# Kernel tuning notes

Hardware: AMD Instinct MI355X
Metric: run time of the kernel (lower is better)

Reference implementation:

```python
import jax, jax.numpy as jnp
import numpy as np


def setup_inputs() -> dict:
    key = jax.random.key(0)
    k1, k2, k3 = jax.random.split(key, 3)
    B, C_in, H, W = 16, 256, 64, 64
    C_out, KH, KW = 256, 3, 3
    x = jax.random.normal(k1, (B, C_in, H, W), dtype=jnp.float32)
    # kaiming-uniform-like scale for realism
    fan_in = C_in * KH * KW
    bound = 1.0 / np.sqrt(fan_in)
    weights = jax.random.normal(k2, (C_out, C_in, KH, KW), dtype=jnp.float32) * bound
    bias = jax.random.uniform(k3, (C_out,), dtype=jnp.float32, minval=-bound, maxval=bound)
    return {"x": x, "weights": weights, "bias": bias}


def reference(x, weights, bias):
    # Conv2dApproximation with approximation_enable=False is an exact conv2d:
    # input is unfolded to [B, C*kh*kw, oh, ow], weights to [C_out, C*kh*kw],
    # and the MultiApp kernel performs the exact MAC (see exact matmul backward).
    # stride=(1,1), padding=(0,0), dilation=(1,1) per init_kwargs.
    out = jax.lax.conv_general_dilated(
        x, weights,
        window_strides=(1, 1),
        padding=((0, 0), (0, 0)),
        rhs_dilation=(1, 1),
        dimension_numbers=("NCHW", "OIHW", "NCHW"),
    )
    return out + bias[None, :, None, None]
```

## Files before the change

### kernel.cpp

```cpp
#include <hip/hip_runtime.h>
#include <stdint.h>

typedef short short8 __attribute__((ext_vector_type(8)));
typedef float f32x4 __attribute__((ext_vector_type(4)));

#define AS1 __attribute__((address_space(1)))
#define AS3 __attribute__((address_space(3)))

__device__ __forceinline__ void gl_lds16(const void* g, void* l) {
  __builtin_amdgcn_global_load_lds((const AS1 unsigned int*)g,
                                   (AS3 unsigned int*)l, 16, 0, 0);
}

__device__ __forceinline__ unsigned short f2bf(float f) {
  union { float f; unsigned int u; } v; v.f = f;
  return (unsigned short)((v.u + (((v.u >> 16) & 1u) + 0x7fffu)) >> 16);
}

__global__ __launch_bounds__(256) void xpose_kernel(const float* __restrict__ x,
                                                    unsigned short* __restrict__ xt) {
  __shared__ float tile[64][68];
  const int bid = blockIdx.x;
  const int cchunk = bid & 3;
  const int y = (bid >> 2) & 63;
  const int b = bid >> 8;
  const int t = threadIdx.x;
  const int ci0 = cchunk * 64;

  const int cc = t >> 2;
  const int xo = (t & 3) * 16;
  const float* src = x + (((size_t)(b * 256 + ci0 + cc) * 64 + y) * 64 + xo);
  float4 v0 = ((const float4*)src)[0];
  float4 v1 = ((const float4*)src)[1];
  float4 v2 = ((const float4*)src)[2];
  float4 v3 = ((const float4*)src)[3];
  *(float4*)&tile[cc][xo + 0]  = v0;
  *(float4*)&tile[cc][xo + 4]  = v1;
  *(float4*)&tile[cc][xo + 8]  = v2;
  *(float4*)&tile[cc][xo + 12] = v3;
  __syncthreads();

  const int xpos = t >> 2;
  const int ccg = (t & 3) * 16;
  unsigned int pk[8];
#pragma unroll
  for (int e = 0; e < 8; ++e) {
    unsigned int lo = f2bf(tile[ccg + 2 * e][xpos]);
    unsigned int hi = f2bf(tile[ccg + 2 * e + 1][xpos]);
    pk[e] = lo | (hi << 16);
  }
  unsigned short* dst = xt + ((size_t)(b * 4096 + y * 64 + xpos) * 256 + ci0 + ccg);
  uint4 w0; w0.x = pk[0]; w0.y = pk[1]; w0.z = pk[2]; w0.w = pk[3];
  uint4 w1; w1.x = pk[4]; w1.y = pk[5]; w1.z = pk[6]; w1.w = pk[7];
  ((uint4*)dst)[0] = w0;
  ((uint4*)dst)[1] = w1;
}

__global__ __launch_bounds__(256) void wpack_kernel(const float* __restrict__ w,
                                                    unsigned short* __restrict__ wrp) {
  const int idx = blockIdx.x * 256 + threadIdx.x;
  const int ci = idx & 255;
  const int co = (idx >> 8) & 255;
  const int p = idx >> 16;
  wrp[idx] = f2bf(w[(size_t)(co * 256 + ci) * 9 + p]);
}

__global__ __launch_bounds__(512, 4) void conv_mfma2(
    const unsigned short* __restrict__ xt,
    const unsigned short* __restrict__ wrp,
    const float* __restrict__ bias,
    float* __restrict__ out) {
  __shared__ unsigned short lds[3 * 12288];

  const int tid = threadIdx.x;
  const int lane = tid & 63;
  const int wv = tid >> 6;
  const int wc = wv & 1;
  const int wp = wv >> 1;
  const int bid = blockIdx.x;
  const int cohalf = bid >> 8;
  const int b = (bid >> 4) & 15;
  const int oh0 = (bid & 15) * 4;
  const int co0 = cohalf * 128;

  const int l2 = lane >> 2;
  const int l3 = lane & 3;
  const int rA = wv * 16 + l2;
  const int slA = l3 ^ ((rA >> 1) & 3);
  const unsigned short* gA = wrp + (size_t)(co0 + rA) * 256 + slA * 8;
  const unsigned short* gB[2];
#pragma unroll
  for (int i = 0; i < 2; ++i) {
    const int r = wv * 32 + i * 16 + l2;
    const int sl = l3 ^ ((r >> 1) & 3);
    const int y = min(oh0 + (r >> 6), 61);
    const int xc = min(r & 63, 61);
    gB[i] = xt + ((size_t)(b * 64 + y) * 64 + xc) * 256 + sl * 8;
  }
  const unsigned ldsA  = wv * 512;
  const unsigned ldsB0 = 4096 + wv * 1024;
  const unsigned ldsB1 = 4096 + wv * 1024 + 512;

  int aoff[4], boff[4];
#pragma unroll
  for (int m = 0; m < 4; ++m) {
    const int row = wc * 64 + m * 16 + (lane & 15);
    const int s = (lane >> 4) ^ ((row >> 1) & 3);
    aoff[m] = row * 32 + s * 8;
  }
#pragma unroll
  for (int n = 0; n < 4; ++n) {
    const int row = wp * 64 + n * 16 + (lane & 15);
    const int s = (lane >> 4) ^ ((row >> 1) & 3);
    boff[n] = 4096 + row * 32 + s * 8;
  }

  auto stage = [&](int kt) {
    const int tap = kt >> 3, chunk = (kt & 7) * 32;
    const int kh = (tap * 11) >> 5, kw = tap - kh * 3;
    unsigned short* base = lds + (kt % 3) * 12288;
    gl_lds16(gA + tap * 65536 + chunk, base + ldsA);
    const int Boff = (kh * 64 + kw) * 256 + chunk;
    gl_lds16(gB[0] + Boff, base + ldsB0);
    gl_lds16(gB[1] + Boff, base + ldsB1);
  };

  f32x4 acc[4][4] = {};

  stage(0);
  stage(1);
  asm volatile("s_waitcnt vmcnt(3)" ::: "memory");
  __builtin_amdgcn_s_barrier();

  for (int kt = 0; kt < 72; ++kt) {
    unsigned short* buf = lds + (kt % 3) * 12288;
    short8 a[4], bb[4];
#pragma unroll
    for (int m = 0; m < 4; ++m) a[m] = *(const short8*)(buf + aoff[m]);
#pragma unroll
    for (int n = 0; n < 4; ++n) bb[n] = *(const short8*)(buf + boff[n]);
    if (kt < 70) stage(kt + 2);
    asm volatile("s_waitcnt lgkmcnt(0)" ::: "memory");
    __builtin_amdgcn_sched_barrier(0);
    __builtin_amdgcn_s_setprio(1);
#pragma unroll
    for (int m = 0; m < 4; ++m)
#pragma unroll
      for (int n = 0; n < 4; ++n)
        acc[m][n] = __builtin_amdgcn_mfma_f32_16x16x32_bf16(a[m], bb[n], acc[m][n], 0, 0, 0);
    __builtin_amdgcn_s_setprio(0);
    if (kt < 70)       asm volatile("s_waitcnt vmcnt(3)" ::: "memory");
    else if (kt == 70) asm volatile("s_waitcnt vmcnt(0)" ::: "memory");
    __builtin_amdgcn_s_barrier();
  }

  const int rb = (lane >> 4) * 4;
  const int colp = lane & 15;
#pragma unroll
  for (int m = 0; m < 4; ++m) {
    const int co = co0 + wc * 64 + m * 16 + rb;
    float bv[4];
#pragma unroll
    for (int j = 0; j < 4; ++j) bv[j] = bias[co + j];
#pragma unroll
    for (int n = 0; n < 4; ++n) {
      const int px = wp * 64 + n * 16 + colp;
      const int prow = px >> 6, ow = px & 63;
      const int oh = oh0 + prow;
      if (ow < 62 && oh < 62) {
#pragma unroll
        for (int j = 0; j < 4; ++j)
          out[((size_t)(b * 256 + co + j) * 62 + oh) * 62 + ow] = acc[m][n][j] + bv[j];
      }
    }
  }
}

__global__ __launch_bounds__(256) void conv_naive(const float* __restrict__ x,
                                                  const float* __restrict__ wgt,
                                                  const float* __restrict__ bias,
                                                  float* __restrict__ out) {
  const size_t idx = (size_t)blockIdx.x * 256 + threadIdx.x;
  if (idx >= (size_t)16 * 256 * 62 * 62) return;
  const int ow = (int)(idx % 62);
  size_t r = idx / 62;
  const int oh = (int)(r % 62); r /= 62;
  const int co = (int)(r % 256);
  const int b = (int)(r / 256);
  float s = bias[co];
  for (int ci = 0; ci < 256; ++ci) {
    const float* xp = x + ((size_t)(b * 256 + ci) * 64 + oh) * 64 + ow;
    const float* wp = wgt + (size_t)(co * 256 + ci) * 9;
#pragma unroll
    for (int kh = 0; kh < 3; ++kh)
#pragma unroll
      for (int kw = 0; kw < 3; ++kw)
        s += xp[kh * 64 + kw] * wp[kh * 3 + kw];
  }
  out[idx] = s;
}

extern "C" void kernel_launch(void* const* d_in, const int* in_sizes, int n_in,
                              void* d_out, int out_size, void* d_ws, size_t ws_size,
                              hipStream_t stream) {
  const float* x = (const float*)d_in[0];
  const float* wgt = (const float*)d_in[1];
  const float* bias = (const float*)d_in[2];
  float* out = (float*)d_out;

  const size_t xt_elems = (size_t)16 * 64 * 64 * 256;
  const size_t wr_elems = (size_t)9 * 256 * 256;
  const size_t need = (xt_elems + wr_elems) * sizeof(unsigned short);

  if (ws_size < need) {
    conv_naive<<<61504, 256, 0, stream>>>(x, wgt, bias, out);
    return;
  }

  unsigned short* xt = (unsigned short*)d_ws;
  unsigned short* wrp = xt + xt_elems;

  xpose_kernel<<<4096, 256, 0, stream>>>(x, xt);
  wpack_kernel<<<2304, 256, 0, stream>>>(wgt, wrp);
  conv_mfma2<<<512, 512, 0, stream>>>(xt, wrp, bias, out);
}
```

Baseline: 107.2 us.

## Enlarge conv GEMM tile to 256x256 with phased double-buffered K loop

Replaces the 128x256-per-block implicit GEMM with a 256-channel by 256-pixel block tile, so each block covers all output channels and the grid halves to 256 blocks. The K loop now steps 64 channels per iteration with two LDS buffers and splits each step into four MFMA phases, interleaving the global-to-LDS loads for the next step across the phases. Blocks are remapped with an XCD-aware tile index. This raises data reuse per LDS byte and removes the duplicate input loads across the two channel halves. In exchange it uses more registers (32 accumulators per wave), more LDS per block, more barriers per step, and only one block per CU.

```diff
diff --git a/kernel.cpp b/kernel.cpp
--- a/kernel.cpp
+++ b/kernel.cpp
@@ -65,112 +65,157 @@
   wrp[idx] = f2bf(w[(size_t)(co * 256 + ci) * 9 + p]);
 }
 
-__global__ __launch_bounds__(512, 4) void conv_mfma2(
+__global__ __launch_bounds__(512, 2) void conv_8ph(
     const unsigned short* __restrict__ xt,
     const unsigned short* __restrict__ wrp,
     const float* __restrict__ bias,
     float* __restrict__ out) {
-  __shared__ unsigned short lds[3 * 12288];
+  __shared__ unsigned short lds[2][32768];
 
   const int tid = threadIdx.x;
   const int lane = tid & 63;
   const int wv = tid >> 6;
-  const int wc = wv & 1;
-  const int wp = wv >> 1;
+  const int wm = wv >> 2;
+  const int wn = wv & 3;
   const int bid = blockIdx.x;
-  const int cohalf = bid >> 8;
-  const int b = (bid >> 4) & 15;
-  const int oh0 = (bid & 15) * 4;
-  const int co0 = cohalf * 128;
-
-  const int l2 = lane >> 2;
-  const int l3 = lane & 3;
-  const int rA = wv * 16 + l2;
-  const int slA = l3 ^ ((rA >> 1) & 3);
-  const unsigned short* gA = wrp + (size_t)(co0 + rA) * 256 + slA * 8;
-  const unsigned short* gB[2];
-#pragma unroll
-  for (int i = 0; i < 2; ++i) {
-    const int r = wv * 32 + i * 16 + l2;
-    const int sl = l3 ^ ((r >> 1) & 3);
-    const int y = min(oh0 + (r >> 6), 61);
-    const int xc = min(r & 63, 61);
-    gB[i] = xt + ((size_t)(b * 64 + y) * 64 + xc) * 256 + sl * 8;
-  }
-  const unsigned ldsA  = wv * 512;
-  const unsigned ldsB0 = 4096 + wv * 1024;
-  const unsigned ldsB1 = 4096 + wv * 1024 + 512;
-
-  int aoff[4], boff[4];
-#pragma unroll
-  for (int m = 0; m < 4; ++m) {
-    const int row = wc * 64 + m * 16 + (lane & 15);
-    const int s = (lane >> 4) ^ ((row >> 1) & 3);
-    aoff[m] = row * 32 + s * 8;
-  }
-#pragma unroll
-  for (int n = 0; n < 4; ++n) {
-    const int row = wp * 64 + n * 16 + (lane & 15);
-    const int s = (lane >> 4) ^ ((row >> 1) & 3);
-    boff[n] = 4096 + row * 32 + s * 8;
-  }
-
-  auto stage = [&](int kt) {
-    const int tap = kt >> 3, chunk = (kt & 7) * 32;
+  const int tile = (bid & 7) * 32 + (bid >> 3);
+  const int b = tile >> 4;
+  const int oh0 = (tile & 15) * 4;
+
+  const int crow = tid >> 3;
+  const int cslot = tid & 7;
+  const int sw = cslot ^ (crow & 7);
+  const unsigned short* gAbase = wrp + (size_t)crow * 256 + sw * 8;
+  const unsigned short* gBbase[4];
+#pragma unroll
+  for (int cb = 0; cb < 4; ++cb) {
+    const int y = min(oh0 + cb, 61);
+    const int x = min(crow, 61);
+    gBbase[cb] = xt + ((size_t)(b * 64 + y) * 64 + x) * 256 + sw * 8;
+  }
+  const unsigned dst_rc = crow * 64 + cslot * 8;
+
+  const int l15 = lane & 15;
+  int s8[2];
+  s8[0] = (((lane >> 4)) ^ (lane & 7)) * 8;
+  s8[1] = (((lane >> 4) + 4) ^ (lane & 7)) * 8;
+  int arow[8], brow[4];
+#pragma unroll
+  for (int a = 0; a < 8; ++a)
+    arow[a] = (wm * 128 + (a >> 2) * 64 + (a & 3) * 16 + l15) * 64;
+#pragma unroll
+  for (int n = 0; n < 4; ++n)
+    brow[n] = 16384 + (wn * 64 + n * 16 + l15) * 64;
+
+  auto stageA = [&](int kt2, int c, unsigned short* bufp) {
+    const int tap = kt2 >> 2, ci0 = (kt2 & 3) * 64;
+    gl_lds16(gAbase + tap * 65536 + c * 16384 + ci0, bufp + c * 4096 + dst_rc);
+  };
+  auto stageB = [&](int kt2, int cb, unsigned short* bufp) {
+    const int tap = kt2 >> 2, ci0 = (kt2 & 3) * 64;
     const int kh = (tap * 11) >> 5, kw = tap - kh * 3;
-    unsigned short* base = lds + (kt % 3) * 12288;
-    gl_lds16(gA + tap * 65536 + chunk, base + ldsA);
-    const int Boff = (kh * 64 + kw) * 256 + chunk;
-    gl_lds16(gB[0] + Boff, base + ldsB0);
-    gl_lds16(gB[1] + Boff, base + ldsB1);
+    gl_lds16(gBbase[cb] + (kh * 64 + kw) * 256 + ci0, bufp + (4 + cb) * 4096 + dst_rc);
   };
 
-  f32x4 acc[4][4] = {};
-
-  stage(0);
-  stage(1);
-  asm volatile("s_waitcnt vmcnt(3)" ::: "memory");
+  f32x4 acc[8][4] = {};
+  unsigned short* buf0 = &lds[0][0];
+  unsigned short* buf1 = &lds[1][0];
+
+  stageA(0, 0, buf0); stageA(0, 2, buf0); stageA(0, 1, buf0); stageA(0, 3, buf0);
+  stageB(0, 2, buf0); stageB(0, 3, buf0); stageB(0, 0, buf0); stageB(0, 1, buf0);
+  stageB(1, 0, buf1); stageB(1, 1, buf1);
+  asm volatile("s_waitcnt vmcnt(2)" ::: "memory");
   __builtin_amdgcn_s_barrier();
 
-  for (int kt = 0; kt < 72; ++kt) {
-    unsigned short* buf = lds + (kt % 3) * 12288;
-    short8 a[4], bb[4];
-#pragma unroll
-    for (int m = 0; m < 4; ++m) a[m] = *(const short8*)(buf + aoff[m]);
-#pragma unroll
-    for (int n = 0; n < 4; ++n) bb[n] = *(const short8*)(buf + boff[n]);
-    if (kt < 70) stage(kt + 2);
-    asm volatile("s_waitcnt lgkmcnt(0)" ::: "memory");
-    __builtin_amdgcn_sched_barrier(0);
-    __builtin_amdgcn_s_setprio(1);
-#pragma unroll
-    for (int m = 0; m < 4; ++m)
-#pragma unroll
-      for (int n = 0; n < 4; ++n)
-        acc[m][n] = __builtin_amdgcn_mfma_f32_16x16x32_bf16(a[m], bb[n], acc[m][n], 0, 0, 0);
-    __builtin_amdgcn_s_setprio(0);
-    if (kt < 70)       asm volatile("s_waitcnt vmcnt(3)" ::: "memory");
-    else if (kt == 70) asm volatile("s_waitcnt vmcnt(0)" ::: "memory");
+  for (int kt = 0; kt < 36; ++kt) {
+    unsigned short* buf = (kt & 1) ? buf1 : buf0;
+    unsigned short* nbuf = (kt & 1) ? buf0 : buf1;
+    short8 a0[4], a1[4], bb[4];
+
+#pragma unroll
+    for (int q = 0; q < 4; ++q) a0[q] = *(const short8*)(buf + arow[q] + s8[0]);
+#pragma unroll
+    for (int n = 0; n < 4; ++n) bb[n] = *(const short8*)(buf + brow[n] + s8[0]);
+    if (kt < 35) { stageA(kt + 1, 0, nbuf); stageA(kt + 1, 2, nbuf); }
+    __builtin_amdgcn_s_barrier();
+    asm volatile("s_waitcnt lgkmcnt(0)" ::: "memory");
+    __builtin_amdgcn_sched_barrier(0);
+    __builtin_amdgcn_s_setprio(1);
+#pragma unroll
+    for (int q = 0; q < 4; ++q)
+#pragma unroll
+      for (int n = 0; n < 4; ++n)
+        acc[q][n] = __builtin_amdgcn_mfma_f32_16x16x32_bf16(a0[q], bb[n], acc[q][n], 0, 0, 0);
+    __builtin_amdgcn_s_setprio(0);
+    __builtin_amdgcn_s_barrier();
+
+#pragma unroll
+    for (int q = 0; q < 4; ++q) a1[q] = *(const short8*)(buf + arow[4 + q] + s8[0]);
+    if (kt < 35) { stageA(kt + 1, 1, nbuf); stageA(kt + 1, 3, nbuf); }
+    __builtin_amdgcn_s_barrier();
+    asm volatile("s_waitcnt lgkmcnt(0)" ::: "memory");
+    __builtin_amdgcn_sched_barrier(0);
+    __builtin_amdgcn_s_setprio(1);
+#pragma unroll
+    for (int q = 0; q < 4; ++q)
+#pragma unroll
+      for (int n = 0; n < 4; ++n)
+        acc[4 + q][n] = __builtin_amdgcn_mfma_f32_16x16x32_bf16(a1[q], bb[n], acc[4 + q][n], 0, 0, 0);
+    __builtin_amdgcn_s_setprio(0);
+    __builtin_amdgcn_s_barrier();
+
+#pragma unroll
+    for (int q = 0; q < 4; ++q) a0[q] = *(const short8*)(buf + arow[q] + s8[1]);
+#pragma unroll
+    for (int n = 0; n < 4; ++n) bb[n] = *(const short8*)(buf + brow[n] + s8[1]);
+    if (kt < 35) { stageB(kt + 1, 2, nbuf); stageB(kt + 1, 3, nbuf); }
+    __builtin_amdgcn_s_barrier();
+    asm volatile("s_waitcnt lgkmcnt(0)" ::: "memory");
+    __builtin_amdgcn_sched_barrier(0);
+    __builtin_amdgcn_s_setprio(1);
+#pragma unroll
+    for (int q = 0; q < 4; ++q)
+#pragma unroll
+      for (int n = 0; n < 4; ++n)
+        acc[q][n] = __builtin_amdgcn_mfma_f32_16x16x32_bf16(a0[q], bb[n], acc[q][n], 0, 0, 0);
+    __builtin_amdgcn_s_setprio(0);
+    __builtin_amdgcn_s_barrier();
+
+#pragma unroll
+    for (int q = 0; q < 4; ++q) a1[q] = *(const short8*)(buf + arow[4 + q] + s8[1]);
+    if (kt < 34) { stageB(kt + 2, 0, buf); stageB(kt + 2, 1, buf); }
+    __builtin_amdgcn_s_barrier();
+    asm volatile("s_waitcnt lgkmcnt(0)" ::: "memory");
+    __builtin_amdgcn_sched_barrier(0);
+    __builtin_amdgcn_s_setprio(1);
+#pragma unroll
+    for (int q = 0; q < 4; ++q)
+#pragma unroll
+      for (int n = 0; n < 4; ++n)
+        acc[4 + q][n] = __builtin_amdgcn_mfma_f32_16x16x32_bf16(a1[q], bb[n], acc[4 + q][n], 0, 0, 0);
+    __builtin_amdgcn_s_setprio(0);
+    if (kt < 34)       asm volatile("s_waitcnt vmcnt(2)" ::: "memory");
+    else if (kt == 34) asm volatile("s_waitcnt vmcnt(0)" ::: "memory");
     __builtin_amdgcn_s_barrier();
   }
 
   const int rb = (lane >> 4) * 4;
   const int colp = lane & 15;
 #pragma unroll
-  for (int m = 0; m < 4; ++m) {
-    const int co = co0 + wc * 64 + m * 16 + rb;
+  for (int a = 0; a < 8; ++a) {
+    const int co = wm * 128 + (a >> 2) * 64 + (a & 3) * 16 + rb;
     float bv[4];
 #pragma unroll
     for (int j = 0; j < 4; ++j) bv[j] = bias[co + j];
 #pragma unroll
     for (int n = 0; n < 4; ++n) {
-      const int px = wp * 64 + n * 16 + colp;
+      const int px = wn * 64 + n * 16 + colp;
       const int prow = px >> 6, ow = px & 63;
       const int oh = oh0 + prow;
       if (ow < 62 && oh < 62) {
 #pragma unroll
         for (int j = 0; j < 4; ++j)
-          out[((size_t)(b * 256 + co + j) * 62 + oh) * 62 + ow] = acc[m][n][j] + bv[j];
+          out[((size_t)(b * 256 + co + j) * 62 + oh) * 62 + ow] = acc[a][n][j] + bv[j];
       }
     }
   }
@@ -222,5 +267,5 @@
 
   xpose_kernel<<<4096, 256, 0, stream>>>(x, xt);
   wpack_kernel<<<2304, 256, 0, stream>>>(wgt, wrp);
-  conv_mfma2<<<512, 512, 0, stream>>>(xt, wrp, bias, out);
-}
+  conv_8ph<<<256, 512, 0, stream>>>(xt, wrp, bias, out);
+}
```

Measured after the change: 97.53 us. 1.1x faster.

## Enlarge conv block tile to all output channels with 4-deep LDS ring

Applied to the files above, without the earlier changes.

Each block now computes all 256 output channels for 256 pixels (previously 128x256), halving the grid to 256 blocks so the input tile is loaded once instead of twice. The LDS is a 4-slot ring, and A and B loads are issued in two phases per k-step, interleaved with two half-MFMA batches and extra barriers. Blocks are also remapped with a swizzled tile index. Each wave holds 8x4 accumulators, which raises register pressure (launch bounds relaxed to 2). With only 256 blocks, occupancy on a 256-CU device drops to one block per CU.

```diff
diff --git a/kernel.cpp b/kernel.cpp
--- a/kernel.cpp
+++ b/kernel.cpp
@@ -65,91 +65,99 @@
   wrp[idx] = f2bf(w[(size_t)(co * 256 + ci) * 9 + p]);
 }
 
-__global__ __launch_bounds__(512, 4) void conv_mfma2(
+__global__ __launch_bounds__(512, 2) void conv_ring4(
     const unsigned short* __restrict__ xt,
     const unsigned short* __restrict__ wrp,
     const float* __restrict__ bias,
     float* __restrict__ out) {
-  __shared__ unsigned short lds[3 * 12288];
+  __shared__ unsigned short lds[4][16384];
 
   const int tid = threadIdx.x;
   const int lane = tid & 63;
   const int wv = tid >> 6;
-  const int wc = wv & 1;
-  const int wp = wv >> 1;
+  const int wm = wv >> 2;
+  const int wn = wv & 3;
   const int bid = blockIdx.x;
-  const int cohalf = bid >> 8;
-  const int b = (bid >> 4) & 15;
-  const int oh0 = (bid & 15) * 4;
-  const int co0 = cohalf * 128;
-
-  const int l2 = lane >> 2;
-  const int l3 = lane & 3;
-  const int rA = wv * 16 + l2;
-  const int slA = l3 ^ ((rA >> 1) & 3);
-  const unsigned short* gA = wrp + (size_t)(co0 + rA) * 256 + slA * 8;
+  const int tile = (bid & 7) * 32 + (bid >> 3);
+  const int b = tile >> 4;
+  const int oh0 = (tile & 15) * 4;
+
+  const int srow = tid >> 2;
+  const int slin = tid & 3;
+  const int sw = slin ^ (srow & 3);
+  const unsigned short* gA = wrp + (size_t)srow * 256 + sw * 8;
   const unsigned short* gB[2];
 #pragma unroll
   for (int i = 0; i < 2; ++i) {
-    const int r = wv * 32 + i * 16 + l2;
-    const int sl = l3 ^ ((r >> 1) & 3);
-    const int y = min(oh0 + (r >> 6), 61);
-    const int xc = min(r & 63, 61);
-    gB[i] = xt + ((size_t)(b * 64 + y) * 64 + xc) * 256 + sl * 8;
-  }
-  const unsigned ldsA  = wv * 512;
-  const unsigned ldsB0 = 4096 + wv * 1024;
-  const unsigned ldsB1 = 4096 + wv * 1024 + 512;
-
-  int aoff[4], boff[4];
-#pragma unroll
-  for (int m = 0; m < 4; ++m) {
-    const int row = wc * 64 + m * 16 + (lane & 15);
-    const int s = (lane >> 4) ^ ((row >> 1) & 3);
-    aoff[m] = row * 32 + s * 8;
-  }
-#pragma unroll
-  for (int n = 0; n < 4; ++n) {
-    const int row = wp * 64 + n * 16 + (lane & 15);
-    const int s = (lane >> 4) ^ ((row >> 1) & 3);
-    boff[n] = 4096 + row * 32 + s * 8;
-  }
-
-  auto stage = [&](int kt) {
-    const int tap = kt >> 3, chunk = (kt & 7) * 32;
+    const int px = i * 128 + srow;
+    const int y = min(oh0 + (px >> 6), 61);
+    const int xc = min(px & 63, 61);
+    gB[i] = xt + ((size_t)(b * 64 + y) * 64 + xc) * 256 + sw * 8;
+  }
+  const unsigned dstA = srow * 32 + slin * 8;
+
+  auto stageA = [&](int kt2) {
+    const int tap = kt2 >> 3, ci0 = (kt2 & 7) * 32;
+    unsigned short* s = &lds[kt2 & 3][0];
+    const unsigned short* g = gA + tap * 65536 + ci0;
+    gl_lds16(g, s + dstA);
+    gl_lds16(g + 128 * 256, s + 4096 + dstA);
+  };
+  auto stageB = [&](int kt2) {
+    const int tap = kt2 >> 3, ci0 = (kt2 & 7) * 32;
     const int kh = (tap * 11) >> 5, kw = tap - kh * 3;
-    unsigned short* base = lds + (kt % 3) * 12288;
-    gl_lds16(gA + tap * 65536 + chunk, base + ldsA);
-    const int Boff = (kh * 64 + kw) * 256 + chunk;
-    gl_lds16(gB[0] + Boff, base + ldsB0);
-    gl_lds16(gB[1] + Boff, base + ldsB1);
+    const int off = (kh * 64 + kw) * 256 + ci0;
+    unsigned short* s = &lds[kt2 & 3][0];
+    gl_lds16(gB[0] + off, s + 8192 + dstA);
+    gl_lds16(gB[1] + off, s + 8192 + 4096 + dstA);
   };
 
-  f32x4 acc[4][4] = {};
-
-  stage(0);
-  stage(1);
-  asm volatile("s_waitcnt vmcnt(3)" ::: "memory");
+  const int l15 = lane & 15;
+  const int fsl = (((lane >> 4)) ^ (l15 & 3)) * 8;
+
+  f32x4 acc[8][4] = {};
+
+  stageA(0); stageB(0);
+  stageA(1); stageB(1);
+  asm volatile("s_waitcnt vmcnt(4)" ::: "memory");
   __builtin_amdgcn_s_barrier();
 
   for (int kt = 0; kt < 72; ++kt) {
-    unsigned short* buf = lds + (kt % 3) * 12288;
-    short8 a[4], bb[4];
-#pragma unroll
-    for (int m = 0; m < 4; ++m) a[m] = *(const short8*)(buf + aoff[m]);
-#pragma unroll
-    for (int n = 0; n < 4; ++n) bb[n] = *(const short8*)(buf + boff[n]);
-    if (kt < 70) stage(kt + 2);
+    const unsigned short* s = &lds[kt & 3][0];
+    short8 af[4], bf[4];
+
+#pragma unroll
+    for (int m = 0; m < 4; ++m)
+      af[m] = *(const short8*)(s + (wm * 128 + m * 16 + l15) * 32 + fsl);
+#pragma unroll
+    for (int n = 0; n < 4; ++n)
+      bf[n] = *(const short8*)(s + 8192 + (wn * 64 + n * 16 + l15) * 32 + fsl);
+    if (kt < 70) stageA(kt + 2);
+    __builtin_amdgcn_s_barrier();
+    __builtin_amdgcn_s_setprio(1);
+#pragma unroll
+    for (int m = 0; m < 4; ++m)
+#pragma unroll
+      for (int n = 0; n < 4; ++n)
+        acc[m][n] = __builtin_amdgcn_mfma_f32_16x16x32_bf16(af[m], bf[n], acc[m][n], 0, 0, 0);
+    __builtin_amdgcn_s_setprio(0);
     asm volatile("s_waitcnt lgkmcnt(0)" ::: "memory");
-    __builtin_amdgcn_sched_barrier(0);
+    __builtin_amdgcn_s_barrier();
+
+#pragma unroll
+    for (int m = 0; m < 4; ++m)
+      af[m] = *(const short8*)(s + (wm * 128 + (4 + m) * 16 + l15) * 32 + fsl);
+    if (kt < 70) stageB(kt + 2);
+    __builtin_amdgcn_s_barrier();
     __builtin_amdgcn_s_setprio(1);
 #pragma unroll
     for (int m = 0; m < 4; ++m)
 #pragma unroll
       for (int n = 0; n < 4; ++n)
-        acc[m][n] = __builtin_amdgcn_mfma_f32_16x16x32_bf16(a[m], bb[n], acc[m][n], 0, 0, 0);
+        acc[4 + m][n] = __builtin_amdgcn_mfma_f32_16x16x32_bf16(af[m], bf[n], acc[4 + m][n], 0, 0, 0);
     __builtin_amdgcn_s_setprio(0);
-    if (kt < 70)       asm volatile("s_waitcnt vmcnt(3)" ::: "memory");
+    asm volatile("s_waitcnt lgkmcnt(0)" ::: "memory");
+    if (kt <= 69)      asm volatile("s_waitcnt vmcnt(4)" ::: "memory");
     else if (kt == 70) asm volatile("s_waitcnt vmcnt(0)" ::: "memory");
     __builtin_amdgcn_s_barrier();
   }
@@ -157,14 +165,14 @@
   const int rb = (lane >> 4) * 4;
   const int colp = lane & 15;
 #pragma unroll
-  for (int m = 0; m < 4; ++m) {
-    const int co = co0 + wc * 64 + m * 16 + rb;
+  for (int m = 0; m < 8; ++m) {
+    const int co = wm * 128 + m * 16 + rb;
     float bv[4];
 #pragma unroll
     for (int j = 0; j < 4; ++j) bv[j] = bias[co + j];
 #pragma unroll
     for (int n = 0; n < 4; ++n) {
-      const int px = wp * 64 + n * 16 + colp;
+      const int px = wn * 64 + n * 16 + colp;
       const int prow = px >> 6, ow = px & 63;
       const int oh = oh0 + prow;
       if (ow < 62 && oh < 62) {
@@ -222,5 +230,5 @@
 
   xpose_kernel<<<4096, 256, 0, stream>>>(x, xt);
   wpack_kernel<<<2304, 256, 0, stream>>>(wgt, wrp);
-  conv_mfma2<<<512, 512, 0, stream>>>(xt, wrp, bias, out);
-}
+  conv_ring4<<<256, 512, 0, stream>>>(xt, wrp, bias, out);
+}
```

Result: faster. 104.7 us (-2.3%).
